# Optimization experiments

Hardware: AMD Instinct MI355X
Metric: run time of the kernel (lower is better)

The kernel has to match this reference:

```python
import jax, jax.numpy as jnp
import numpy as np

N_NODES = 50000


def gcn_conv(x, W, b, row, col, n):
    """PyG GCNConv with default add_self_loops=True, normalize=True.
    out[i] = sum_{e: col[e]=i} d^-1/2[row[e]] d^-1/2[i] * (x@W)[row[e]]
             + d^-1[i]*(x@W)[i] + b,  where d = in-degree + 1 (self-loop).
    """
    x_lin = x @ W                                   # [n, out_ch]
    ones = jnp.ones(row.shape[0], dtype=x.dtype)
    deg = jax.ops.segment_sum(ones, col, num_segments=n) + 1.0  # self-loop
    dinv = jax.lax.rsqrt(deg)                       # deg >= 1, safe
    norm = dinv[row] * dinv[col]                    # [E]
    msg = norm[:, None] * x_lin[row]                # [E, out_ch]
    agg = jax.ops.segment_sum(msg, col, num_segments=n)
    self_term = (dinv * dinv)[:, None] * x_lin      # self-loop contribution
    return agg + self_term + b


def setup_inputs() -> dict:
    key = jax.random.key(0)
    ks = jax.random.split(key, 10)
    in_ch, hid, out_ch = 128, 256, 64
    E = 800000
    x = jax.random.normal(ks[0], (N_NODES, in_ch), dtype=jnp.float32)
    edge_attr = jax.random.normal(ks[1], (E, 8), dtype=jnp.float32)  # unused by forward
    edge_index = jax.random.randint(ks[2], (2, E), 0, N_NODES, dtype=jnp.int64)
    def glorot(k, fan_in, fan_out):
        s = float(np.sqrt(6.0 / (fan_in + fan_out)))
        return jax.random.uniform(k, (fan_in, fan_out), jnp.float32, -s, s)
    return {
        "x": x,
        "edge_attr": edge_attr,
        "edge_index": edge_index,
        "W1": glorot(ks[3], in_ch, hid), "b1": jnp.zeros((hid,), jnp.float32),
        "W2": glorot(ks[4], hid, hid),  "b2": jnp.zeros((hid,), jnp.float32),
        "W3": glorot(ks[5], hid, out_ch), "b3": jnp.zeros((out_ch,), jnp.float32),
    }


def reference(x, edge_attr, edge_index, W1, b1, W2, b2, W3, b3):
    n = x.shape[0]
    row, col = edge_index[0], edge_index[1]
    h = jax.nn.sigmoid(gcn_conv(x, W1, b1, row, col, n))
    h = jax.nn.sigmoid(gcn_conv(h, W2, b2, row, col, n))
    # dropout(p=0.1) in eval mode is identity
    return gcn_conv(h, W3, b3, row, col, n)
```

## Files before the change

### kernel.cpp

```cpp
#include <hip/hip_runtime.h>
#include <hip/hip_bf16.h>

typedef __bf16 bf16x8_t __attribute__((ext_vector_type(8)));
typedef float f32x4_t __attribute__((ext_vector_type(4)));
typedef float f32x2_t __attribute__((ext_vector_type(2)));

__device__ __forceinline__ float bits2f(unsigned int u) {
    union { unsigned int u; float f; } c; c.u = u; return c.f;
}
__device__ __forceinline__ unsigned short f2bf_bits(float f) {
    __hip_bfloat16 h = __float2bfloat16(f);
    return __builtin_bit_cast(unsigned short, h);
}
__device__ __forceinline__ f32x2_t unpack_bf2(unsigned int u) {
    return (f32x2_t){bits2f(u << 16), bits2f(u & 0xffff0000u)};
}

__global__ void sentinel_fill(float* __restrict__ out, int n) {
    int i = blockIdx.x * blockDim.x + threadIdx.x;
    if (i < n) out[i] = 100.0f;
}

__global__ void detect_ei(const unsigned int* __restrict__ ei, int* __restrict__ flags) {
    int lane = threadIdx.x;
    int cz = 0;
    #pragma unroll
    for (int j = 0; j < 4; ++j) {
        int idx = lane * 4 + j;
        cz += (ei[2 * idx + 1] == 0u);
    }
    #pragma unroll
    for (int off = 32; off; off >>= 1) cz += __shfl_down(cz, off);
    if (lane == 0) flags[0] = (cz > 200);
}


__global__ void count_rank_dual2(const int* __restrict__ ei, int* __restrict__ cnt,
                                 int* __restrict__ rank, int* __restrict__ c32,
                                 int* __restrict__ r32, int E, int M,
                                 const int* __restrict__ flags) {
    int e = blockIdx.x * blockDim.x + threadIdx.x;
    if (e < E) {
        int r, c;
        if (flags[0]) { r = ei[2 * e]; c = ei[2 * E + 2 * e]; }
        else          { r = ei[e];     c = ei[E + e]; }
        c32[e] = c;
        r32[e] = r;
        int rk = 0;
        if ((unsigned)c < (unsigned)M) rk = atomicAdd(&cnt[c], 1);
        rank[e] = rk;
    }
}

__global__ void scan_blocks(const int* __restrict__ cnt, int* __restrict__ excl,
                            int* __restrict__ bsum, int n) {
    int tid = threadIdx.x;
    int i = blockIdx.x * 256 + tid;
    int lane = tid & 63, wv = tid >> 6;
    __shared__ int ws[4];
    int v = (i < n) ? cnt[i] : 0;
    int s = v;
    #pragma unroll
    for (int off = 1; off < 64; off <<= 1) {
        int t = __shfl_up(s, off);
        if (lane >= off) s += t;
    }
    if (lane == 63) ws[wv] = s;
    __syncthreads();
    if (tid == 0) { int a = 0; for (int q = 0; q < 4; ++q) { int t = ws[q]; ws[q] = a; a += t; } }
    __syncthreads();
    int ex = s - v + ws[wv];
    if (i < n) excl[i] = ex;
    if (tid == 255) bsum[blockIdx.x] = ex + v;
}

__global__ void scan_bsums(const int* __restrict__ bsum, int* __restrict__ boff,
                           int nb, int* __restrict__ colptr, int n) {
    int tid = threadIdx.x, lane = tid & 63, wv = tid >> 6;
    __shared__ int ws[4];
    __shared__ int carry;
    if (tid == 0) carry = 0;
    __syncthreads();
    for (int base = 0; base < nb; base += 256) {
        int i = base + tid;
        int v = (i < nb) ? bsum[i] : 0;
        int s = v;
        #pragma unroll
        for (int off = 1; off < 64; off <<= 1) {
            int t = __shfl_up(s, off);
            if (lane >= off) s += t;
        }
        if (lane == 63) ws[wv] = s;
        __syncthreads();
        if (tid == 0) { int a = carry; for (int q = 0; q < 4; ++q) { int t = ws[q]; ws[q] = a; a += t; } carry = a; }
        __syncthreads();
        int ex = s - v + ws[wv];
        if (i < nb) boff[i] = ex;
        __syncthreads();
    }
    if (tid == 0) colptr[n] = carry;
}

__global__ void scan_add_dinv(const int* __restrict__ excl, const int* __restrict__ boff,
                              const int* __restrict__ cnt, int* __restrict__ colptr,
                              float* __restrict__ dinv, int n) {
    int i = blockIdx.x * 256 + threadIdx.x;
    if (i < n) {
        colptr[i] = excl[i] + boff[blockIdx.x];
        dinv[i] = rsqrtf((float)cnt[i] + 1.0f);
    }
}

__global__ void fill_csr_part2(const int* __restrict__ c32, const int* __restrict__ r32,
                               const int* __restrict__ colptr, const int* __restrict__ rank,
                               int* __restrict__ esrc, int E, int M, int psz) {
    int part = blockIdx.x & 7;
    int e = (blockIdx.x >> 3) * 256 + threadIdx.x;
    int lo = part * psz;
    int hi = lo + psz; if (hi > M) hi = M;
    if (e < E) {
        int c = c32[e];
        if (c >= lo && c < hi) {
            int r = r32[e];
            if ((unsigned)r < (unsigned)M) {
                int p = colptr[c] + rank[e];
                if ((unsigned)p < (unsigned)E) esrc[p] = r;
            }
        }
    }
}

__global__ void prep_fused(const float* __restrict__ x, const float* __restrict__ dinv,
                           unsigned char* __restrict__ xs8,
                           const float* __restrict__ W1, const float* __restrict__ W2,
                           const float* __restrict__ W3,
                           unsigned short* __restrict__ Wt1, unsigned short* __restrict__ Wt2,
                           unsigned short* __restrict__ Wt3,
                           int M, int nps) {
    if ((int)blockIdx.x < nps) {
        int i = blockIdx.x * 256 + threadIdx.x;
        if (i < M * 32) {
            int row = i >> 5;
            float dv = dinv[row];
            float4 v = *(const float4*)(x + (size_t)i * 4);
            unsigned u = __builtin_amdgcn_cvt_pk_fp8_f32(v.x * dv, v.y * dv, 0, false);
            u = __builtin_amdgcn_cvt_pk_fp8_f32(v.z * dv, v.w * dv, u, true);
            *(unsigned*)(xs8 + (size_t)i * 4) = u;
        }
    } else {
        int i = ((int)blockIdx.x - nps) * 256 + threadIdx.x;
        if (i < 32768) {
            int k = i >> 8, n = i & 255;
            Wt1[n * 128 + k] = f2bf_bits(W1[i]);
        } else if (i < 32768 + 65536) {
            int j = i - 32768;
            int k = j >> 8, n = j & 255;
            Wt2[n * 256 + k] = f2bf_bits(W2[j]);
        } else if (i < 114688) {
            int j = i - 98304;
            int k = j >> 6, n = j & 63;
            Wt3[n * 256 + k] = f2bf_bits(W3[j]);
        }
    }
}

template<int K, int BN, int NTOT, int EPI>
__global__ __launch_bounds__(256) void gemm_tile(
    const __bf16* __restrict__ A,
    const unsigned short* __restrict__ Bt,
    const float* __restrict__ dinv,
    const float* __restrict__ bias,
    void* __restrict__ Y,
    int M)
{
    constexpr int KS = (K > 128) ? 128 : K;
    constexpr int KP = KS + 8;
    constexpr int NT = BN / 2 / 16;
    __shared__ unsigned short Bs[BN * KP];

    const int tid  = threadIdx.x;
    const int lane = tid & 63;
    const int wave = tid >> 6;
    const int wm   = wave >> 1;
    const int wn   = wave & 1;
    const int quad = lane >> 4;
    const int l16  = lane & 15;
    const int n0   = blockIdx.y * BN;

    int mrow[4];
#pragma unroll
    for (int mt = 0; mt < 4; ++mt) {
        int r = blockIdx.x * 128 + wm * 64 + mt * 16 + l16;
        mrow[mt] = (r < M) ? r : (M - 1);
    }

    f32x4_t acc[4][NT];
#pragma unroll
    for (int mt = 0; mt < 4; ++mt)
#pragma unroll
        for (int t = 0; t < NT; ++t) acc[mt][t] = (f32x4_t){0.f, 0.f, 0.f, 0.f};

    const unsigned short* BsW = &Bs[(wn * (BN / 2)) * KP];

    for (int kh = 0; kh < K; kh += KS) {
        constexpr int CH = BN * KS / 8;
        for (int idx = tid; idx < CH; idx += 256) {
            int n  = idx / (KS / 8);
            int k8 = idx - n * (KS / 8);
            uint4 v = *(const uint4*)(Bt + (size_t)(n0 + n) * K + kh + k8 * 8);
            *(uint4*)&Bs[n * KP + k8 * 8] = v;
        }
        __syncthreads();

#pragma unroll
        for (int kc = 0; kc < KS; kc += 32) {
            bf16x8_t a[4], b[NT];
#pragma unroll
            for (int mt = 0; mt < 4; ++mt)
                a[mt] = *(const bf16x8_t*)(A + (size_t)mrow[mt] * K + kh + kc + quad * 8);
#pragma unroll
            for (int t = 0; t < NT; ++t)
                b[t] = *(const bf16x8_t*)&BsW[(t * 16 + l16) * KP + kc + quad * 8];
#pragma unroll
            for (int mt = 0; mt < 4; ++mt)
#pragma unroll
                for (int t = 0; t < NT; ++t)
                    acc[mt][t] = __builtin_amdgcn_mfma_f32_16x16x32_bf16(a[mt], b[t], acc[mt][t], 0, 0, 0);
        }
        if (kh + KS < K) __syncthreads();
    }

    float bv[NT];
    if constexpr (EPI == 1) {
#pragma unroll
        for (int t = 0; t < NT; ++t)
            bv[t] = bias[n0 + wn * (BN / 2) + t * 16 + l16];
    }

#pragma unroll
    for (int mt = 0; mt < 4; ++mt) {
        int rowbase = blockIdx.x * 128 + wm * 64 + mt * 16 + quad * 4;
#pragma unroll
        for (int r = 0; r < 4; ++r) {
            int rrow = rowbase + r;
            if (rrow < M) {
                if constexpr (EPI == 0) {
                    float dv = dinv[rrow];
#pragma unroll
                    for (int t = 0; t < NT; ++t) {
                        int ccol = n0 + wn * (BN / 2) + t * 16 + l16;
                        ((__hip_bfloat16*)Y)[(size_t)rrow * NTOT + ccol] =
                            __float2bfloat16(acc[mt][t][r] * dv);
                    }
                } else if constexpr (EPI == 1) {
#pragma unroll
                    for (int t = 0; t < NT; ++t) {
                        int ccol = n0 + wn * (BN / 2) + t * 16 + l16;
                        float o = acc[mt][t][r] + bv[t];
                        o = 1.f / (1.f + __expf(-o));
                        ((__hip_bfloat16*)Y)[(size_t)rrow * NTOT + ccol] = __float2bfloat16(o);
                    }
                } else {
                    float dv = dinv[rrow];
#pragma unroll
                    for (int t = 0; t < NT; ++t) {
                        int ccol = n0 + wn * (BN / 2) + t * 16 + l16;
                        float o = acc[mt][t][r] * dv;
                        int pk = __builtin_amdgcn_cvt_pk_fp8_f32(o, o, 0, false);
                        size_t choff = (size_t)(ccol >> 7) * ((size_t)M * 128)
                                     + (size_t)rrow * 128 + (ccol & 127);
                        ((unsigned char*)Y)[choff] = (unsigned char)(pk & 0xff);
                    }
                }
            }
        }
    }
}

__global__ __launch_bounds__(256) void aggregate_fp8_x2b(
    const unsigned char* __restrict__ Y8c,
    const int* __restrict__ colptr,
    const int* __restrict__ esrc,
    const float* __restrict__ dinv,
    const float* __restrict__ bias,
    unsigned short* __restrict__ H,
    int M, int Etot, int ga)
{
    const int lane = threadIdx.x & 63;
    const int wave = threadIdx.x >> 6;
    const int l4 = lane & 15;
    const int g4 = lane >> 4;

    int s8 = blockIdx.x & 7;
    int chunk = s8 >> 2;
    int grp = (blockIdx.x >> 3) * 4 + (s8 & 3);
    if (grp >= ga) return;
    int node = grp * 4 + wave;
    if (node >= M) return;

    int s = colptr[node];
    int e = colptr[node + 1];
    if (s < 0) s = 0;
    if (e > Etot) e = Etot;
    if (e < s) e = s;
    int n = e - s;

    const char* Yb = (const char*)(Y8c + (size_t)chunk * ((size_t)M * 128));
    const unsigned lb = (unsigned)(l4 * 8);

    uint2 su = {0u, 0u};
    if (g4 == 0) su = *(const uint2*)(Yb + ((unsigned)node) * 128u + lb);

    f32x2_t a0 = {0.f, 0.f}, a1 = {0.f, 0.f}, a2 = {0.f, 0.f}, a3 = {0.f, 0.f};

    auto gat = [&](uint2* u, int base) {
        u[0] = *(const uint2*)(Yb + ((unsigned)esrc[s + base + g4]) * 128u + lb);
        u[1] = *(const uint2*)(Yb + ((unsigned)esrc[s + base + 4 + g4]) * 128u + lb);
    };
    auto acc = [&](const uint2* u) {
        #pragma unroll
        for (int k = 0; k < 2; ++k) {
            a0 += __builtin_amdgcn_cvt_pk_f32_fp8(u[k].x, false);
            a1 += __builtin_amdgcn_cvt_pk_f32_fp8(u[k].x, true);
            a2 += __builtin_amdgcn_cvt_pk_f32_fp8(u[k].y, false);
            a3 += __builtin_amdgcn_cvt_pk_f32_fp8(u[k].y, true);
        }
    };

    uint2 ua[2], ub[2];
    int NB = n >> 3;
    if (NB > 0) {
        gat(ua, 0);
        int i = 1;
        for (; i + 1 < NB; i += 2) {
            gat(ub, i << 3); acc(ua);
            gat(ua, (i + 1) << 3); acc(ub);
        }
        if (i < NB) { gat(ub, i << 3); acc(ua); acc(ub); }
        else acc(ua);
    }
    for (int t = NB << 3; t < n; t += 4) {
        if (t + g4 < n) {
            uint2 u = *(const uint2*)(Yb + ((unsigned)esrc[s + t + g4]) * 128u + lb);
            a0 += __builtin_amdgcn_cvt_pk_f32_fp8(u.x, false);
            a1 += __builtin_amdgcn_cvt_pk_f32_fp8(u.x, true);
            a2 += __builtin_amdgcn_cvt_pk_f32_fp8(u.y, false);
            a3 += __builtin_amdgcn_cvt_pk_f32_fp8(u.y, true);
        }
    }
    if (g4 == 0) {
        a0 += __builtin_amdgcn_cvt_pk_f32_fp8(su.x, false);
        a1 += __builtin_amdgcn_cvt_pk_f32_fp8(su.x, true);
        a2 += __builtin_amdgcn_cvt_pk_f32_fp8(su.y, false);
        a3 += __builtin_amdgcn_cvt_pk_f32_fp8(su.y, true);
    }

    #pragma unroll
    for (int off = 16; off < 64; off <<= 1) {
        a0[0] += __shfl_xor(a0[0], off); a0[1] += __shfl_xor(a0[1], off);
        a1[0] += __shfl_xor(a1[0], off); a1[1] += __shfl_xor(a1[1], off);
        a2[0] += __shfl_xor(a2[0], off); a2[1] += __shfl_xor(a2[1], off);
        a3[0] += __shfl_xor(a3[0], off); a3[1] += __shfl_xor(a3[1], off);
    }

    if (g4 == 0) {
        float dv = dinv[node];
        int chb = chunk * 128 + l4 * 8;
        float4 b0 = *(const float4*)(bias + chb);
        float4 b1 = *(const float4*)(bias + chb + 4);
        float o[8];
        o[0] = a0[0] * dv + b0.x; o[1] = a0[1] * dv + b0.y;
        o[2] = a1[0] * dv + b0.z; o[3] = a1[1] * dv + b0.w;
        o[4] = a2[0] * dv + b1.x; o[5] = a2[1] * dv + b1.y;
        o[6] = a3[0] * dv + b1.z; o[7] = a3[1] * dv + b1.w;
        #pragma unroll
        for (int k = 0; k < 8; ++k) o[k] = 1.f / (1.f + __expf(-o[k]));
        uint4 st;
        st.x = (unsigned)f2bf_bits(o[0]) | ((unsigned)f2bf_bits(o[1]) << 16);
        st.y = (unsigned)f2bf_bits(o[2]) | ((unsigned)f2bf_bits(o[3]) << 16);
        st.z = (unsigned)f2bf_bits(o[4]) | ((unsigned)f2bf_bits(o[5]) << 16);
        st.w = (unsigned)f2bf_bits(o[6]) | ((unsigned)f2bf_bits(o[7]) << 16);
        *(uint4*)(H + (size_t)node * 256 + chb) = st;
    }
}

__global__ __launch_bounds__(256) void aggregate_xs8b(
    const unsigned char* __restrict__ X8,
    const int* __restrict__ colptr,
    const int* __restrict__ esrc,
    const float* __restrict__ dinv,
    unsigned short* __restrict__ xa,
    int M, int Etot)
{
    const int lane = threadIdx.x & 63;
    const int wave = threadIdx.x >> 6;
    const int l4 = lane & 15;
    const int g4 = lane >> 4;
    int node = blockIdx.x * 4 + wave;
    if (node >= M) return;

    int s = colptr[node];
    int e = colptr[node + 1];
    if (s < 0) s = 0;
    if (e > Etot) e = Etot;
    if (e < s) e = s;
    int n = e - s;

    const char* Yb = (const char*)X8;
    const unsigned lb = (unsigned)(l4 * 8);

    uint2 su = {0u, 0u};
    if (g4 == 0) su = *(const uint2*)(Yb + ((unsigned)node) * 128u + lb);

    f32x2_t a0 = {0.f, 0.f}, a1 = {0.f, 0.f}, a2 = {0.f, 0.f}, a3 = {0.f, 0.f};

    auto gat = [&](uint2* u, int base) {
        u[0] = *(const uint2*)(Yb + ((unsigned)esrc[s + base + g4]) * 128u + lb);
        u[1] = *(const uint2*)(Yb + ((unsigned)esrc[s + base + 4 + g4]) * 128u + lb);
    };
    auto acc = [&](const uint2* u) {
        #pragma unroll
        for (int k = 0; k < 2; ++k) {
            a0 += __builtin_amdgcn_cvt_pk_f32_fp8(u[k].x, false);
            a1 += __builtin_amdgcn_cvt_pk_f32_fp8(u[k].x, true);
            a2 += __builtin_amdgcn_cvt_pk_f32_fp8(u[k].y, false);
            a3 += __builtin_amdgcn_cvt_pk_f32_fp8(u[k].y, true);
        }
    };

    uint2 ua[2], ub[2];
    int NB = n >> 3;
    if (NB > 0) {
        gat(ua, 0);
        int i = 1;
        for (; i + 1 < NB; i += 2) {
            gat(ub, i << 3); acc(ua);
            gat(ua, (i + 1) << 3); acc(ub);
        }
        if (i < NB) { gat(ub, i << 3); acc(ua); acc(ub); }
        else acc(ua);
    }
    for (int t = NB << 3; t < n; t += 4) {
        if (t + g4 < n) {
            uint2 u = *(const uint2*)(Yb + ((unsigned)esrc[s + t + g4]) * 128u + lb);
            a0 += __builtin_amdgcn_cvt_pk_f32_fp8(u.x, false);
            a1 += __builtin_amdgcn_cvt_pk_f32_fp8(u.x, true);
            a2 += __builtin_amdgcn_cvt_pk_f32_fp8(u.y, false);
            a3 += __builtin_amdgcn_cvt_pk_f32_fp8(u.y, true);
        }
    }
    if (g4 == 0) {
        a0 += __builtin_amdgcn_cvt_pk_f32_fp8(su.x, false);
        a1 += __builtin_amdgcn_cvt_pk_f32_fp8(su.x, true);
        a2 += __builtin_amdgcn_cvt_pk_f32_fp8(su.y, false);
        a3 += __builtin_amdgcn_cvt_pk_f32_fp8(su.y, true);
    }

    #pragma unroll
    for (int off = 16; off < 64; off <<= 1) {
        a0[0] += __shfl_xor(a0[0], off); a0[1] += __shfl_xor(a0[1], off);
        a1[0] += __shfl_xor(a1[0], off); a1[1] += __shfl_xor(a1[1], off);
        a2[0] += __shfl_xor(a2[0], off); a2[1] += __shfl_xor(a2[1], off);
        a3[0] += __shfl_xor(a3[0], off); a3[1] += __shfl_xor(a3[1], off);
    }

    if (g4 == 0) {
        float dv = dinv[node];
        uint4 st;
        st.x = (unsigned)f2bf_bits(a0[0] * dv) | ((unsigned)f2bf_bits(a0[1] * dv) << 16);
        st.y = (unsigned)f2bf_bits(a1[0] * dv) | ((unsigned)f2bf_bits(a1[1] * dv) << 16);
        st.z = (unsigned)f2bf_bits(a2[0] * dv) | ((unsigned)f2bf_bits(a2[1] * dv) << 16);
        st.w = (unsigned)f2bf_bits(a3[0] * dv) | ((unsigned)f2bf_bits(a3[1] * dv) << 16);
        *(uint4*)(xa + (size_t)node * 128 + l4 * 8) = st;
    }
}

__global__ __launch_bounds__(256) void aggregate_bf16_64_v5(
    const unsigned short* __restrict__ Yin,
    const int* __restrict__ colptr,
    const int* __restrict__ esrc,
    const float* __restrict__ dinv,
    const float* __restrict__ bias,
    float* __restrict__ out,
    int M, int Etot)
{
    const int lane = threadIdx.x & 63;
    const int wave = threadIdx.x >> 6;
    const int l4 = lane & 15;
    const int g4 = lane >> 4;
    int node = blockIdx.x * 4 + wave;
    if (node >= M) return;

    int s = colptr[node];
    int e = colptr[node + 1];
    if (s < 0) s = 0;
    if (e > Etot) e = Etot;
    if (e < s) e = s;
    int n = e - s;

    const char* Yb = (const char*)Yin;
    const unsigned lb = (unsigned)(l4 * 8);

    uint2 su = {0u, 0u};
    if (g4 == 0) su = *(const uint2*)(Yb + ((unsigned)node) * 128u + lb);

    f32x2_t a0 = {0.f, 0.f}, a1 = {0.f, 0.f};

    auto gat = [&](uint2* u, int base) {
        u[0] = *(const uint2*)(Yb + ((unsigned)esrc[s + base + g4]) * 128u + lb);
        u[1] = *(const uint2*)(Yb + ((unsigned)esrc[s + base + 4 + g4]) * 128u + lb);
    };
    auto acc = [&](const uint2* u) {
        #pragma unroll
        for (int k = 0; k < 2; ++k) {
            a0 += unpack_bf2(u[k].x);
            a1 += unpack_bf2(u[k].y);
        }
    };

    uint2 ua[2], ub[2];
    int NB = n >> 3;
    if (NB > 0) {
        gat(ua, 0);
        int i = 1;
        for (; i + 1 < NB; i += 2) {
            gat(ub, i << 3); acc(ua);
            gat(ua, (i + 1) << 3); acc(ub);
        }
        if (i < NB) { gat(ub, i << 3); acc(ua); acc(ub); }
        else acc(ua);
    }
    for (int t = NB << 3; t < n; t += 4) {
        if (t + g4 < n) {
            uint2 u = *(const uint2*)(Yb + ((unsigned)esrc[s + t + g4]) * 128u + lb);
            a0 += unpack_bf2(u.x);
            a1 += unpack_bf2(u.y);
        }
    }
    if (g4 == 0) {
        a0 += unpack_bf2(su.x);
        a1 += unpack_bf2(su.y);
    }

    #pragma unroll
    for (int off = 16; off < 64; off <<= 1) {
        a0[0] += __shfl_xor(a0[0], off); a0[1] += __shfl_xor(a0[1], off);
        a1[0] += __shfl_xor(a1[0], off); a1[1] += __shfl_xor(a1[1], off);
    }

    if (g4 == 0) {
        float dv = dinv[node];
        float4 bv = *(const float4*)(bias + l4 * 4);
        float4 st;
        st.x = a0[0] * dv + bv.x;
        st.y = a0[1] * dv + bv.y;
        st.z = a1[0] * dv + bv.z;
        st.w = a1[1] * dv + bv.w;
        *(float4*)(out + (size_t)node * 64 + l4 * 4) = st;
    }
}


extern "C" void kernel_launch(void* const* d_in, const int* in_sizes, int n_in,
                              void* d_out, int out_size, void* d_ws, size_t ws_size,
                              hipStream_t stream)
{
    int iEI = 2, iW1 = 3, iB1 = 4, iW2 = 5, iB2 = 6, iW3 = 7, iB3 = 8;
    if (n_in == 8) { iEI = 1; iW1 = 2; iB1 = 3; iW2 = 4; iB2 = 5; iW3 = 6; iB3 = 7; }

    const float* x  = (const float*)d_in[0];
    const int* ei   = (const int*)d_in[iEI];
    const float* W1 = (const float*)d_in[iW1];
    const float* b1 = (const float*)d_in[iB1];
    const float* W2 = (const float*)d_in[iW2];
    const float* b2 = (const float*)d_in[iB2];
    const float* W3 = (const float*)d_in[iW3];
    const float* b3 = (const float*)d_in[iB3];

    const int M = in_sizes[0] / 128;
    const int E = in_sizes[iEI] / 2;
    const int NB = (M + 255) / 256;
    const int PSZ = (M + 7) / 8;

    auto rnd = [](size_t b) { return (b + 255) & ~(size_t)255; };
    size_t needed = rnd(64 * 4)
                  + rnd((size_t)M * 4) * 2
                  + rnd((size_t)(M + 1) * 4)
                  + rnd((size_t)M * 4)
                  + rnd((size_t)(NB + 1) * 4) * 2
                  + rnd((size_t)E * 4) * 4
                  + rnd((size_t)256 * 128 * 2)
                  + rnd((size_t)256 * 256 * 2)
                  + rnd((size_t)64 * 256 * 2)
                  + rnd((size_t)M * 256 * 2) * 2;
    if (ws_size < needed) {
        sentinel_fill<<<(out_size + 255) / 256, 256, 0, stream>>>((float*)d_out, out_size);
        return;
    }

    char* p = (char*)d_ws;
    auto alloc = [&](size_t bytes) {
        char* r = p;
        p += (bytes + 255) & ~(size_t)255;
        return r;
    };
    int* flags  = (int*)alloc(64 * 4);
    float* dinv = (float*)alloc((size_t)M * 4);
    int* cnt    = (int*)alloc((size_t)M * 4);
    int* colptr = (int*)alloc((size_t)(M + 1) * 4);
    int* excl   = (int*)alloc((size_t)M * 4);
    int* bsum   = (int*)alloc((size_t)(NB + 1) * 4);
    int* boff   = (int*)alloc((size_t)(NB + 1) * 4);
    int* esrc   = (int*)alloc((size_t)E * 4);
    int* rank   = (int*)alloc((size_t)E * 4);
    int* c32    = (int*)alloc((size_t)E * 4);
    int* r32    = (int*)alloc((size_t)E * 4);
    unsigned short* Wt1 = (unsigned short*)alloc((size_t)256 * 128 * 2);
    unsigned short* Wt2 = (unsigned short*)alloc((size_t)256 * 256 * 2);
    unsigned short* Wt3 = (unsigned short*)alloc((size_t)64 * 256 * 2);
    __hip_bfloat16* ybuf = (__hip_bfloat16*)alloc((size_t)M * 256 * 2);
    __hip_bfloat16* hbuf = (__hip_bfloat16*)alloc((size_t)M * 256 * 2);

    unsigned char* xs8 = (unsigned char*)ybuf;
    unsigned short* xa = (unsigned short*)ybuf + (size_t)M * 128;
    unsigned char*  y8 = (unsigned char*)ybuf;

    detect_ei<<<1, 64, 0, stream>>>((const unsigned int*)ei, flags);

    hipMemsetAsync(cnt, 0, (size_t)M * 4, stream);
    count_rank_dual2<<<(E + 255) / 256, 256, 0, stream>>>(ei, cnt, rank, c32, r32, E, M, flags);
    scan_blocks<<<NB, 256, 0, stream>>>(cnt, excl, bsum, M);
    scan_bsums<<<1, 256, 0, stream>>>(bsum, boff, NB, colptr, M);
    scan_add_dinv<<<NB, 256, 0, stream>>>(excl, boff, cnt, colptr, dinv, M);
    fill_csr_part2<<<((E + 255) / 256) * 8, 256, 0, stream>>>(
        c32, r32, colptr, rank, esrc, E, M, PSZ);

    int gmb = (M + 127) / 128;
    int ga  = (M + 3) / 4;
    int nps = (M * 32 + 255) / 256;
    int nsup = (ga + 3) / 4;

    prep_fused<<<nps + 448, 256, 0, stream>>>(
        x, dinv, xs8, W1, W2, W3, Wt1, Wt2, Wt3, M, nps);

    aggregate_xs8b<<<ga, 256, 0, stream>>>(
        xs8, colptr, esrc, dinv, xa, M, E);
    gemm_tile<128, 128, 256, 1><<<dim3(gmb, 2), 256, 0, stream>>>(
        (const __bf16*)xa, Wt1, dinv, b1, hbuf, M);
    gemm_tile<256, 128, 256, 2><<<dim3(gmb, 2), 256, 0, stream>>>(
        (const __bf16*)hbuf, Wt2, dinv, b2, y8, M);
    aggregate_fp8_x2b<<<nsup * 8, 256, 0, stream>>>(
        y8, colptr, esrc, dinv, b2, (unsigned short*)hbuf, M, E, ga);
    gemm_tile<256, 64, 64, 0><<<dim3(gmb, 1), 256, 0, stream>>>(
        (const __bf16*)hbuf, Wt3, dinv, b3, ybuf, M);
    aggregate_bf16_64_v5<<<ga, 256, 0, stream>>>(
        (const unsigned short*)ybuf, colptr, esrc, dinv, b3, (float*)d_out, M, E);
}
```

Baseline: 344.6 us.

## Use row-major fp8 layout and whole-wave-per-node aggregation; fuse memset into detect kernel

The layer-2 GEMM now writes its fp8 output row-major (256 bytes per node) rather than split into two 128-column chunks. The aggregation kernel is rewritten so one wave covers all 256 channels of a node, with each lane gathering 4 bytes per neighbour, eight neighbours in flight. This removes the cross-lane shuffle reduction and the dual-chunk block mapping, at the cost of narrower per-lane loads and more index loads per lane. Separately, the edge-format detection and the zeroing of the count buffer are merged into one kernel launch, replacing a memset plus a tiny launch.

```diff
diff --git a/kernel.cpp b/kernel.cpp
--- a/kernel.cpp
+++ b/kernel.cpp
@@ -21,17 +21,25 @@
     if (i < n) out[i] = 100.0f;
 }
 
-__global__ void detect_ei(const unsigned int* __restrict__ ei, int* __restrict__ flags) {
-    int lane = threadIdx.x;
-    int cz = 0;
-    #pragma unroll
-    for (int j = 0; j < 4; ++j) {
-        int idx = lane * 4 + j;
-        cz += (ei[2 * idx + 1] == 0u);
-    }
-    #pragma unroll
-    for (int off = 32; off; off >>= 1) cz += __shfl_down(cz, off);
-    if (lane == 0) flags[0] = (cz > 200);
+__global__ void init_combo(const unsigned int* __restrict__ ei, int* __restrict__ flags,
+                           int* __restrict__ cnt, int M) {
+    if (blockIdx.x == 0) {
+        if (threadIdx.x < 64) {
+            int lane = threadIdx.x;
+            int cz = 0;
+            #pragma unroll
+            for (int j = 0; j < 4; ++j) {
+                int idx = lane * 4 + j;
+                cz += (ei[2 * idx + 1] == 0u);
+            }
+            #pragma unroll
+            for (int off = 32; off; off >>= 1) cz += __shfl_down(cz, off);
+            if (lane == 0) flags[0] = (cz > 200);
+        }
+    } else {
+        int i = (blockIdx.x - 1) * 256 + threadIdx.x;
+        if (i < M) cnt[i] = 0;
+    }
 }
 
 
@@ -267,9 +275,7 @@
                         int ccol = n0 + wn * (BN / 2) + t * 16 + l16;
                         float o = acc[mt][t][r] * dv;
                         int pk = __builtin_amdgcn_cvt_pk_fp8_f32(o, o, 0, false);
-                        size_t choff = (size_t)(ccol >> 7) * ((size_t)M * 128)
-                                     + (size_t)rrow * 128 + (ccol & 127);
-                        ((unsigned char*)Y)[choff] = (unsigned char)(pk & 0xff);
+                        ((unsigned char*)Y)[(size_t)rrow * NTOT + ccol] = (unsigned char)(pk & 0xff);
                     }
                 }
             }
@@ -277,25 +283,18 @@
     }
 }
 
-__global__ __launch_bounds__(256) void aggregate_fp8_x2b(
-    const unsigned char* __restrict__ Y8c,
+__global__ __launch_bounds__(256) void aggregate_fp8_v4(
+    const unsigned char* __restrict__ Y8,
     const int* __restrict__ colptr,
     const int* __restrict__ esrc,
     const float* __restrict__ dinv,
     const float* __restrict__ bias,
     unsigned short* __restrict__ H,
-    int M, int Etot, int ga)
+    int M, int Etot)
 {
     const int lane = threadIdx.x & 63;
     const int wave = threadIdx.x >> 6;
-    const int l4 = lane & 15;
-    const int g4 = lane >> 4;
-
-    int s8 = blockIdx.x & 7;
-    int chunk = s8 >> 2;
-    int grp = (blockIdx.x >> 3) * 4 + (s8 & 3);
-    if (grp >= ga) return;
-    int node = grp * 4 + wave;
+    int node = blockIdx.x * 4 + wave;
     if (node >= M) return;
 
     int s = colptr[node];
@@ -305,83 +304,71 @@
     if (e < s) e = s;
     int n = e - s;
 
-    const char* Yb = (const char*)(Y8c + (size_t)chunk * ((size_t)M * 128));
-    const unsigned lb = (unsigned)(l4 * 8);
-
-    uint2 su = {0u, 0u};
-    if (g4 == 0) su = *(const uint2*)(Yb + ((unsigned)node) * 128u + lb);
-
-    f32x2_t a0 = {0.f, 0.f}, a1 = {0.f, 0.f}, a2 = {0.f, 0.f}, a3 = {0.f, 0.f};
-
-    auto gat = [&](uint2* u, int base) {
-        u[0] = *(const uint2*)(Yb + ((unsigned)esrc[s + base + g4]) * 128u + lb);
-        u[1] = *(const uint2*)(Yb + ((unsigned)esrc[s + base + 4 + g4]) * 128u + lb);
+    const char* Yb = (const char*)Y8;
+    const unsigned lb = (unsigned)(lane * 4);
+
+    unsigned su = *(const unsigned*)(Yb + (((unsigned)node) << 8) + lb);
+
+    f32x2_t a0 = {0.f, 0.f}, a1 = {0.f, 0.f};
+
+    auto gather8 = [&](unsigned* u, int base) {
+        #pragma unroll
+        for (int k = 0; k < 8; ++k) {
+            unsigned off = (((unsigned)esrc[s + base + k]) << 8) + lb;
+            u[k] = *(const unsigned*)(Yb + off);
+        }
     };
-    auto acc = [&](const uint2* u) {
+    auto acc8 = [&](const unsigned* u) {
         #pragma unroll
-        for (int k = 0; k < 2; ++k) {
-            a0 += __builtin_amdgcn_cvt_pk_f32_fp8(u[k].x, false);
-            a1 += __builtin_amdgcn_cvt_pk_f32_fp8(u[k].x, true);
-            a2 += __builtin_amdgcn_cvt_pk_f32_fp8(u[k].y, false);
-            a3 += __builtin_amdgcn_cvt_pk_f32_fp8(u[k].y, true);
+        for (int k = 0; k < 8; ++k) {
+            a0 += __builtin_amdgcn_cvt_pk_f32_fp8(u[k], false);
+            a1 += __builtin_amdgcn_cvt_pk_f32_fp8(u[k], true);
         }
     };
 
-    uint2 ua[2], ub[2];
+    unsigned ua[8], ub[8];
     int NB = n >> 3;
     if (NB > 0) {
-        gat(ua, 0);
+        gather8(ua, 0);
         int i = 1;
         for (; i + 1 < NB; i += 2) {
-            gat(ub, i << 3); acc(ua);
-            gat(ua, (i + 1) << 3); acc(ub);
-        }
-        if (i < NB) { gat(ub, i << 3); acc(ua); acc(ub); }
-        else acc(ua);
-    }
-    for (int t = NB << 3; t < n; t += 4) {
-        if (t + g4 < n) {
-            uint2 u = *(const uint2*)(Yb + ((unsigned)esrc[s + t + g4]) * 128u + lb);
-            a0 += __builtin_amdgcn_cvt_pk_f32_fp8(u.x, false);
-            a1 += __builtin_amdgcn_cvt_pk_f32_fp8(u.x, true);
-            a2 += __builtin_amdgcn_cvt_pk_f32_fp8(u.y, false);
-            a3 += __builtin_amdgcn_cvt_pk_f32_fp8(u.y, true);
-        }
-    }
-    if (g4 == 0) {
-        a0 += __builtin_amdgcn_cvt_pk_f32_fp8(su.x, false);
-        a1 += __builtin_amdgcn_cvt_pk_f32_fp8(su.x, true);
-        a2 += __builtin_amdgcn_cvt_pk_f32_fp8(su.y, false);
-        a3 += __builtin_amdgcn_cvt_pk_f32_fp8(su.y, true);
-    }
-
-    #pragma unroll
-    for (int off = 16; off < 64; off <<= 1) {
-        a0[0] += __shfl_xor(a0[0], off); a0[1] += __shfl_xor(a0[1], off);
-        a1[0] += __shfl_xor(a1[0], off); a1[1] += __shfl_xor(a1[1], off);
-        a2[0] += __shfl_xor(a2[0], off); a2[1] += __shfl_xor(a2[1], off);
-        a3[0] += __shfl_xor(a3[0], off); a3[1] += __shfl_xor(a3[1], off);
-    }
-
-    if (g4 == 0) {
-        float dv = dinv[node];
-        int chb = chunk * 128 + l4 * 8;
-        float4 b0 = *(const float4*)(bias + chb);
-        float4 b1 = *(const float4*)(bias + chb + 4);
-        float o[8];
-        o[0] = a0[0] * dv + b0.x; o[1] = a0[1] * dv + b0.y;
-        o[2] = a1[0] * dv + b0.z; o[3] = a1[1] * dv + b0.w;
-        o[4] = a2[0] * dv + b1.x; o[5] = a2[1] * dv + b1.y;
-        o[6] = a3[0] * dv + b1.z; o[7] = a3[1] * dv + b1.w;
-        #pragma unroll
-        for (int k = 0; k < 8; ++k) o[k] = 1.f / (1.f + __expf(-o[k]));
-        uint4 st;
-        st.x = (unsigned)f2bf_bits(o[0]) | ((unsigned)f2bf_bits(o[1]) << 16);
-        st.y = (unsigned)f2bf_bits(o[2]) | ((unsigned)f2bf_bits(o[3]) << 16);
-        st.z = (unsigned)f2bf_bits(o[4]) | ((unsigned)f2bf_bits(o[5]) << 16);
-        st.w = (unsigned)f2bf_bits(o[6]) | ((unsigned)f2bf_bits(o[7]) << 16);
-        *(uint4*)(H + (size_t)node * 256 + chb) = st;
-    }
+            gather8(ub, i << 3);
+            acc8(ua);
+            gather8(ua, (i + 1) << 3);
+            acc8(ub);
+        }
+        if (i < NB) {
+            gather8(ub, i << 3);
+            acc8(ua);
+            acc8(ub);
+        } else {
+            acc8(ua);
+        }
+    }
+    #pragma unroll 2
+    for (int t = NB << 3; t < n; ++t) {
+        unsigned off = (((unsigned)esrc[s + t]) << 8) + lb;
+        unsigned u = *(const unsigned*)(Yb + off);
+        a0 += __builtin_amdgcn_cvt_pk_f32_fp8(u, false);
+        a1 += __builtin_amdgcn_cvt_pk_f32_fp8(u, true);
+    }
+    a0 += __builtin_amdgcn_cvt_pk_f32_fp8(su, false);
+    a1 += __builtin_amdgcn_cvt_pk_f32_fp8(su, true);
+
+    float dv = dinv[node];
+    float4 bv = *(const float4*)(bias + lane * 4);
+    float o0 = a0[0] * dv + bv.x;
+    float o1 = a0[1] * dv + bv.y;
+    float o2 = a1[0] * dv + bv.z;
+    float o3 = a1[1] * dv + bv.w;
+    o0 = 1.f / (1.f + __expf(-o0));
+    o1 = 1.f / (1.f + __expf(-o1));
+    o2 = 1.f / (1.f + __expf(-o2));
+    o3 = 1.f / (1.f + __expf(-o3));
+    uint2 st;
+    st.x = (unsigned)f2bf_bits(o0) | ((unsigned)f2bf_bits(o1) << 16);
+    st.y = (unsigned)f2bf_bits(o2) | ((unsigned)f2bf_bits(o3) << 16);
+    *(uint2*)(H + (size_t)node * 256 + lane * 4) = st;
 }
 
 __global__ __launch_bounds__(256) void aggregate_xs8b(
@@ -625,9 +612,7 @@
     unsigned short* xa = (unsigned short*)ybuf + (size_t)M * 128;
     unsigned char*  y8 = (unsigned char*)ybuf;
 
-    detect_ei<<<1, 64, 0, stream>>>((const unsigned int*)ei, flags);
-
-    hipMemsetAsync(cnt, 0, (size_t)M * 4, stream);
+    init_combo<<<NB + 1, 256, 0, stream>>>((const unsigned int*)ei, flags, cnt, M);
     count_rank_dual2<<<(E + 255) / 256, 256, 0, stream>>>(ei, cnt, rank, c32, r32, E, M, flags);
     scan_blocks<<<NB, 256, 0, stream>>>(cnt, excl, bsum, M);
     scan_bsums<<<1, 256, 0, stream>>>(bsum, boff, NB, colptr, M);
@@ -638,7 +623,6 @@
     int gmb = (M + 127) / 128;
     int ga  = (M + 3) / 4;
     int nps = (M * 32 + 255) / 256;
-    int nsup = (ga + 3) / 4;
 
     prep_fused<<<nps + 448, 256, 0, stream>>>(
         x, dinv, xs8, W1, W2, W3, Wt1, Wt2, Wt3, M, nps);
@@ -649,8 +633,8 @@
         (const __bf16*)xa, Wt1, dinv, b1, hbuf, M);
     gemm_tile<256, 128, 256, 2><<<dim3(gmb, 2), 256, 0, stream>>>(
         (const __bf16*)hbuf, Wt2, dinv, b2, y8, M);
-    aggregate_fp8_x2b<<<nsup * 8, 256, 0, stream>>>(
-        y8, colptr, esrc, dinv, b2, (unsigned short*)hbuf, M, E, ga);
+    aggregate_fp8_v4<<<ga, 256, 0, stream>>>(
+        y8, colptr, esrc, dinv, b2, (unsigned short*)hbuf, M, E);
     gemm_tile<256, 64, 64, 0><<<dim3(gmb, 1), 256, 0, stream>>>(
         (const __bf16*)hbuf, Wt3, dinv, b3, ybuf, M);
     aggregate_bf16_64_v5<<<ga, 256, 0, stream>>>(
```

Result: faster. 325.4 us (-5.6%).
